# Performance work log

Measured on AMD Instinct MI355X. Metric: run time of the kernel, lower is better.

Reference implementation:

```python
import jax, jax.numpy as jnp
import numpy as np

B, N, D = 16, 1024, 128


def setup_inputs() -> dict:
    key = jax.random.key(0)
    ks = jax.random.split(key, 12)
    x = jax.random.normal(ks[0], (B, N, D), dtype=jnp.float32)
    # binary symmetric-ish adjacency mask (0/1 floats)
    adj = jax.random.randint(ks[1], (B, N, N), 0, 2).astype(jnp.float32)
    Ww = jax.random.normal(ks[2], (D, D), dtype=jnp.float32) * 0.05
    Wb = jax.random.normal(ks[3], (D,), dtype=jnp.float32) * 0.05
    A = jax.random.normal(ks[4], (D, D), dtype=jnp.float32) * 0.05
    wi_u = jax.random.normal(ks[5], (D,), dtype=jnp.float32) * 0.05
    wi_x = jax.random.normal(ks[6], (D,), dtype=jnp.float32) * 0.05
    wf_u = jax.random.normal(ks[7], (D,), dtype=jnp.float32) * 0.05
    wf_x = jax.random.normal(ks[8], (D,), dtype=jnp.float32) * 0.05
    wo_u = jax.random.normal(ks[9], (D,), dtype=jnp.float32) * 0.05
    wo_x = jax.random.normal(ks[10], (D,), dtype=jnp.float32) * 0.05
    return {"x": x, "adj": adj, "Ww": Ww, "Wb": Wb, "A": A,
            "wi_u": wi_u, "wi_x": wi_x, "wf_u": wf_u, "wf_x": wf_x,
            "wo_u": wo_u, "wo_x": wo_x}


def reference(x, adj, Ww, Wb, A, wi_u, wi_x, wf_u, wf_x, wo_u, wo_x):
    # h = W(x): [B,N,D]
    h = jnp.einsum('bnf,df->bnd', x, Ww) + Wb
    # e[b,j,k] = (h A) . h  -> symmetrized dense scores [B,N,N]
    e = jnp.einsum('bjl,bkl->bjk', jnp.einsum('bjd,dl->bjl', h, A), h)
    e = e + jnp.swapaxes(e, 1, 2)
    # masked softmax over axis=1 (columns), then re-mask by adj
    scores = jnp.where(adj > 0, e, 0.0)
    attention = jax.nn.softmax(scores, axis=1) * adj
    # aggregation
    h_prime = jax.nn.relu(jnp.einsum('bij,bjk->bik', attention, h))
    # LSTM-style gates: scalar per node, broadcast over features
    ic = jax.nn.sigmoid(h_prime @ wi_u + x @ wi_x)[..., None]
    fc = jax.nn.sigmoid(h_prime @ wf_u + x @ wf_x)[..., None]
    oc = jax.nn.sigmoid(h_prime @ wo_u + x @ wo_x)[..., None]
    return oc * jnp.tanh(ic * h_prime + fc * x)
```

## Files before the change

kernel.cpp:

```cpp
#include <hip/hip_runtime.h>


#define B_ 16
#define N_ 1024
#define D_ 128

typedef __attribute__((ext_vector_type(8))) short bf16x8;
typedef __attribute__((ext_vector_type(4))) float f32x4;

__device__ __forceinline__ unsigned short f2b(float f) {
    union { float f; unsigned int i; } v; v.f = f;
    unsigned int x = v.i;
    return (unsigned short)((x + 0x7fffu + ((x >> 16) & 1u)) >> 16);
}
__device__ __forceinline__ float clamp60(float v) {
    return fminf(fmaxf(v, -60.f), 60.f);
}
__device__ __forceinline__ bf16x8 load8f(const float* p) {
    float4 a = *reinterpret_cast<const float4*>(p);
    float4 b = *reinterpret_cast<const float4*>(p + 4);
    bf16x8 v;
    v[0] = (short)f2b(a.x); v[1] = (short)f2b(a.y);
    v[2] = (short)f2b(a.z); v[3] = (short)f2b(a.w);
    v[4] = (short)f2b(b.x); v[5] = (short)f2b(b.y);
    v[6] = (short)f2b(b.z); v[7] = (short)f2b(b.w);
    return v;
}

__global__ __launch_bounds__(256) void k0_w2t(
    const float* __restrict__ Ww, const float* __restrict__ Wb,
    const float* __restrict__ A, unsigned short* __restrict__ WwB,
    unsigned short* __restrict__ W2T, float* __restrict__ wbA) {
    int t = blockIdx.x * 256 + threadIdx.x;
    int l = t >> 7, f = t & 127;
    float acc = 0.f;
    for (int d = 0; d < 128; ++d)
        acc += A[d * 128 + l] * Ww[d * 128 + f];
    W2T[l * 128 + f] = f2b(acc);
    WwB[t] = f2b(Ww[t]);
    if (blockIdx.x == 0 && threadIdx.x < 128) {
        float s = 0.f;
        for (int d = 0; d < 128; ++d) s += Wb[d] * A[d * 128 + threadIdx.x];
        wbA[threadIdx.x] = s;
    }
}

__global__ __launch_bounds__(256) void kmask(
    const float* __restrict__ adj, unsigned long long* __restrict__ maskJ) {
    int w = threadIdx.x >> 6, lane = threadIdx.x & 63;
    size_t base = ((size_t)blockIdx.x * 4 + w) * 256;
    unsigned long long w0 = __ballot(adj[base + 0 * 64 + lane] > 0.f);
    unsigned long long w1 = __ballot(adj[base + 1 * 64 + lane] > 0.f);
    unsigned long long w2 = __ballot(adj[base + 2 * 64 + lane] > 0.f);
    unsigned long long w3 = __ballot(adj[base + 3 * 64 + lane] > 0.f);
    unsigned long long o = lane == 0 ? w0 : lane == 1 ? w1 : lane == 2 ? w2 : w3;
    if (lane < 4) maskJ[(base >> 6) + lane] = o;
}

__global__ __launch_bounds__(256) void k1_hu(
    const float* __restrict__ x, const unsigned short* __restrict__ WwB,
    const float* __restrict__ Wb, const unsigned short* __restrict__ W2T,
    const float* __restrict__ wbA,
    unsigned short* __restrict__ h, unsigned short* __restrict__ u,
    unsigned short* __restrict__ hT) {
    __shared__ unsigned short lds[16][128];
    int w = threadIdx.x >> 6, lane = threadIdx.x & 63;
    int c = lane & 15, q = lane >> 4;
    int rowbase = blockIdx.x * 16;
    int b = rowbase >> 10;
    int n0 = rowbase & 1023;

    bf16x8 xa[4];
    const float* xrow = x + (size_t)(rowbase + c) * 128;
#pragma unroll
    for (int ks = 0; ks < 4; ++ks)
        xa[ks] = load8f(xrow + ks * 32 + q * 8);

#pragma unroll
    for (int tt = 0; tt < 2; ++tt) {
        int t = w * 2 + tt;
        f32x4 acch = {0.f, 0.f, 0.f, 0.f};
        f32x4 accu = {0.f, 0.f, 0.f, 0.f};
        const unsigned short* wwrow = WwB + (t * 16 + c) * 128;
        const unsigned short* w2row = W2T + (t * 16 + c) * 128;
#pragma unroll
        for (int ks = 0; ks < 4; ++ks) {
            bf16x8 bw = *reinterpret_cast<const bf16x8*>(wwrow + ks * 32 + q * 8);
            bf16x8 b2 = *reinterpret_cast<const bf16x8*>(w2row + ks * 32 + q * 8);
            acch = __builtin_amdgcn_mfma_f32_16x16x32_bf16(xa[ks], bw, acch, 0, 0, 0);
            accu = __builtin_amdgcn_mfma_f32_16x16x32_bf16(xa[ks], b2, accu, 0, 0, 0);
        }
        float wb = Wb[t * 16 + c];
        float ub = wbA[t * 16 + c];
#pragma unroll
        for (int r = 0; r < 4; ++r) {
            int row = rowbase + q * 4 + r;
            unsigned short hv = f2b(acch[r] + wb);
            unsigned short uv = f2b(accu[r] + ub);
            h[(size_t)row * 128 + t * 16 + c] = hv;
            u[(size_t)row * 128 + t * 16 + c] = uv;
            lds[q * 4 + r][t * 16 + c] = hv;
        }
    }
    __syncthreads();
    int tid = threadIdx.x;
    if (tid < 128) {
        int d = tid;
        unsigned int p[8];
#pragma unroll
        for (int k = 0; k < 8; ++k) {
            unsigned int v0 = lds[2 * k][d], v1 = lds[2 * k + 1][d];
            p[k] = v0 | (v1 << 16);
        }
        size_t basehT = ((size_t)(b * 128 + d)) * 1024 + n0;
        uint4* dst = reinterpret_cast<uint4*>(hT + basehT);
        dst[0] = make_uint4(p[0], p[1], p[2], p[3]);
        dst[1] = make_uint4(p[4], p[5], p[6], p[7]);
    }
}


__global__ __launch_bounds__(256) void k2_scores(
    const unsigned short* __restrict__ h, const unsigned short* __restrict__ u,
    const unsigned long long* __restrict__ maskJ,
    float* __restrict__ att, float* __restrict__ colpart) {
    __shared__ unsigned long long lmask[16][16];
    int w = threadIdx.x >> 6, lane = threadIdx.x & 63;
    int c = lane & 15, q = lane >> 4;
    int b = blockIdx.x >> 6;
    int iblk = blockIdx.x & 63;
    int i0 = iblk * 16;
    const unsigned short* hb = h + (size_t)b * N_ * D_;
    const unsigned short* ub = u + (size_t)b * N_ * D_;

    lmask[threadIdx.x >> 4][threadIdx.x & 15] =
        maskJ[(size_t)(b * 1024 + i0 + (threadIdx.x >> 4)) * 16 + (threadIdx.x & 15)];
    __syncthreads();

    bf16x8 Au[4], Ah[4];
#pragma unroll
    for (int ks = 0; ks < 4; ++ks) {
        Au[ks] = *reinterpret_cast<const bf16x8*>(ub + (i0 + c) * 128 + ks * 32 + q * 8);
        Ah[ks] = *reinterpret_cast<const bf16x8*>(hb + (i0 + c) * 128 + ks * 32 + q * 8);
    }
    float* attrow = att + ((size_t)(b * 1024 + i0)) * 1024;
    float* cprow = colpart + ((size_t)(b * 64 + iblk)) * 1024;

    int jt0 = w * 16;
    bf16x8 Bh[2][4], Bu[2][4];
#pragma unroll
    for (int ks = 0; ks < 4; ++ks) {
        Bh[0][ks] = *reinterpret_cast<const bf16x8*>(hb + (jt0 * 16 + c) * 128 + ks * 32 + q * 8);
        Bu[0][ks] = *reinterpret_cast<const bf16x8*>(ub + (jt0 * 16 + c) * 128 + ks * 32 + q * 8);
    }
#pragma unroll
    for (int t = 0; t < 16; ++t) {
        int jt = jt0 + t, j0 = jt * 16;
        int cur = t & 1, nxt = cur ^ 1;
        if (t < 15) {
            int jn = (jt + 1) * 16;
#pragma unroll
            for (int ks = 0; ks < 4; ++ks) {
                Bh[nxt][ks] = *reinterpret_cast<const bf16x8*>(hb + (jn + c) * 128 + ks * 32 + q * 8);
                Bu[nxt][ks] = *reinterpret_cast<const bf16x8*>(ub + (jn + c) * 128 + ks * 32 + q * 8);
            }
        }
        f32x4 a1 = {0.f, 0.f, 0.f, 0.f};
        f32x4 a2 = {0.f, 0.f, 0.f, 0.f};
#pragma unroll
        for (int ks = 0; ks < 4; ++ks) {
            a1 = __builtin_amdgcn_mfma_f32_16x16x32_bf16(Au[ks], Bh[cur][ks], a1, 0, 0, 0);
            a2 = __builtin_amdgcn_mfma_f32_16x16x32_bf16(Ah[ks], Bu[cur][ks], a2, 0, 0, 0);
        }
        int wd = jt >> 2, sh = (jt & 3) * 16;
        float colp = 0.f;
#pragma unroll
        for (int r = 0; r < 4; ++r) {
            float e = a1[r] + a2[r];
            bool m = (lmask[q * 4 + r][wd] >> (sh + c)) & 1ull;
            float ex = m ? __expf(clamp60(e)) : 0.f;
            colp += m ? ex : 1.0f;
            attrow[(size_t)(q * 4 + r) * 1024 + j0 + c] = ex;
        }
        colp += __shfl_xor(colp, 16, 64);
        colp += __shfl_xor(colp, 32, 64);
        if (q == 0) cprow[j0 + c] = colp;
    }
}

__global__ __launch_bounds__(256) void k2b_recip(
    const float* __restrict__ colpart, float* __restrict__ rl0) {
    int g = blockIdx.x * 256 + threadIdx.x;
    int b = g >> 10, j = g & 1023;
    float s = 0.f;
    const float* p = colpart + (size_t)b * 64 * 1024 + j;
    for (int ib = 0; ib < 64; ++ib) s += p[(size_t)ib * 1024];
    rl0[g] = 1.0f / s;
}

__global__ __launch_bounds__(256) void k3_gemm(
    const float* __restrict__ att, const float* __restrict__ rl0,
    const unsigned short* __restrict__ hT, const float* __restrict__ x,
    const float* __restrict__ wi_u, const float* __restrict__ wi_x,
    const float* __restrict__ wf_u, const float* __restrict__ wf_x,
    const float* __restrict__ wo_u, const float* __restrict__ wo_x,
    float* __restrict__ out) {
    __shared__ float red[4][16][129];
    int w = threadIdx.x >> 6, lane = threadIdx.x & 63;
    int c = lane & 15, q = lane >> 4;
    int b = blockIdx.x >> 6;
    int i0 = (blockIdx.x & 63) * 16;
    const float* attrow = att + ((size_t)(b * 1024 + i0 + c)) * 1024;
    const unsigned short* hTb = hT + (size_t)b * 128 * 1024;
    const float* rl0b = rl0 + b * 1024;

    f32x4 hp[8];
#pragma unroll
    for (int t = 0; t < 8; ++t) hp[t] = (f32x4){0.f, 0.f, 0.f, 0.f};

#pragma unroll
    for (int tt = 0; tt < 8; ++tt) {
        int jp = w * 8 + tt;
        int jb = jp * 32 + q * 8;
        float4 e0 = *reinterpret_cast<const float4*>(attrow + jb);
        float4 e1 = *reinterpret_cast<const float4*>(attrow + jb + 4);
        float4 r0 = *reinterpret_cast<const float4*>(rl0b + jb);
        float4 r1 = *reinterpret_cast<const float4*>(rl0b + jb + 4);
        bf16x8 a;
        a[0] = (short)f2b(e0.x * r0.x); a[1] = (short)f2b(e0.y * r0.y);
        a[2] = (short)f2b(e0.z * r0.z); a[3] = (short)f2b(e0.w * r0.w);
        a[4] = (short)f2b(e1.x * r1.x); a[5] = (short)f2b(e1.y * r1.y);
        a[6] = (short)f2b(e1.z * r1.z); a[7] = (short)f2b(e1.w * r1.w);
#pragma unroll
        for (int t = 0; t < 8; ++t) {
            bf16x8 bt = *reinterpret_cast<const bf16x8*>(
                hTb + (size_t)(t * 16 + c) * 1024 + jp * 32 + q * 8);
            hp[t] = __builtin_amdgcn_mfma_f32_16x16x32_bf16(a, bt, hp[t], 0, 0, 0);
        }
    }

#pragma unroll
    for (int t = 0; t < 8; ++t)
#pragma unroll
        for (int r = 0; r < 4; ++r)
            red[w][q * 4 + r][t * 16 + c] = hp[t][r];
    __syncthreads();
    if (w != 0) return;

#pragma unroll
    for (int t = 0; t < 8; ++t)
#pragma unroll
        for (int r = 0; r < 4; ++r)
            hp[t][r] = red[0][q * 4 + r][t * 16 + c] + red[1][q * 4 + r][t * 16 + c]
                     + red[2][q * 4 + r][t * 16 + c] + red[3][q * 4 + r][t * 16 + c];

    float xv[8][4];
#pragma unroll
    for (int t = 0; t < 8; ++t)
#pragma unroll
        for (int r = 0; r < 4; ++r) {
            hp[t][r] = fmaxf(hp[t][r], 0.f);
            xv[t][r] = x[(size_t)(b * 1024 + i0 + q * 4 + r) * 128 + t * 16 + c];
        }
    float wiu[8], wix[8], wfu[8], wfx[8], wou[8], wox[8];
#pragma unroll
    for (int t = 0; t < 8; ++t) {
        wiu[t] = wi_u[t * 16 + c]; wix[t] = wi_x[t * 16 + c];
        wfu[t] = wf_u[t * 16 + c]; wfx[t] = wf_x[t * 16 + c];
        wou[t] = wo_u[t * 16 + c]; wox[t] = wo_x[t * 16 + c];
    }
#pragma unroll
    for (int r = 0; r < 4; ++r) {
        float zi = 0.f, zf = 0.f, zo = 0.f;
#pragma unroll
        for (int t = 0; t < 8; ++t) {
            zi += hp[t][r] * wiu[t] + xv[t][r] * wix[t];
            zf += hp[t][r] * wfu[t] + xv[t][r] * wfx[t];
            zo += hp[t][r] * wou[t] + xv[t][r] * wox[t];
        }
        zi += __shfl_xor(zi, 1, 64); zi += __shfl_xor(zi, 2, 64);
        zi += __shfl_xor(zi, 4, 64); zi += __shfl_xor(zi, 8, 64);
        zf += __shfl_xor(zf, 1, 64); zf += __shfl_xor(zf, 2, 64);
        zf += __shfl_xor(zf, 4, 64); zf += __shfl_xor(zf, 8, 64);
        zo += __shfl_xor(zo, 1, 64); zo += __shfl_xor(zo, 2, 64);
        zo += __shfl_xor(zo, 4, 64); zo += __shfl_xor(zo, 8, 64);
        float ic = 1.f / (1.f + __expf(-zi));
        float fc = 1.f / (1.f + __expf(-zf));
        float oc = 1.f / (1.f + __expf(-zo));
#pragma unroll
        for (int t = 0; t < 8; ++t) {
            float zz = ic * hp[t][r] + fc * xv[t][r];
            float th = 1.f - 2.f / (__expf(2.f * zz) + 1.f);
            out[(size_t)(b * 1024 + i0 + q * 4 + r) * 128 + t * 16 + c] = oc * th;
        }
    }
}

__global__ __launch_bounds__(256) void k2_stats(
    const unsigned short* __restrict__ h, const unsigned short* __restrict__ u,
    const unsigned long long* __restrict__ maskJ, float* __restrict__ rl0) {
    int w = threadIdx.x >> 6, lane = threadIdx.x & 63;
    int c = lane & 15, q = lane >> 4;
    int b = blockIdx.x >> 6;
    int j0 = (blockIdx.x & 63) * 16;
    const unsigned short* hb = h + (size_t)b * N_ * D_;
    const unsigned short* ub = u + (size_t)b * N_ * D_;

    bf16x8 Bh[4], Bu[4];
#pragma unroll
    for (int ks = 0; ks < 4; ++ks) {
        Bh[ks] = *reinterpret_cast<const bf16x8*>(hb + (j0 + c) * 128 + ks * 32 + q * 8);
        Bu[ks] = *reinterpret_cast<const bf16x8*>(ub + (j0 + c) * 128 + ks * 32 + q * 8);
    }
    float colsum = 0.f;
    const unsigned long long* mrow = maskJ + (size_t)b * 1024 * 16 + (j0 >> 6);
    int jb = j0 & 63;

    for (int it = w; it < 64; it += 4) {
        int i0 = it * 16;
        f32x4 acc = {0.f, 0.f, 0.f, 0.f};
#pragma unroll
        for (int ks = 0; ks < 4; ++ks) {
            bf16x8 au = *reinterpret_cast<const bf16x8*>(ub + (i0 + c) * 128 + ks * 32 + q * 8);
            bf16x8 ah = *reinterpret_cast<const bf16x8*>(hb + (i0 + c) * 128 + ks * 32 + q * 8);
            acc = __builtin_amdgcn_mfma_f32_16x16x32_bf16(au, Bh[ks], acc, 0, 0, 0);
            acc = __builtin_amdgcn_mfma_f32_16x16x32_bf16(ah, Bu[ks], acc, 0, 0, 0);
        }
#pragma unroll
        for (int r = 0; r < 4; ++r) {
            int i = i0 + q * 4 + r;
            unsigned long long mword = mrow[(size_t)i * 16];
            bool m = (mword >> (jb + c)) & 1ull;
            colsum += m ? __expf(clamp60(acc[r])) : 1.0f;
        }
    }
    colsum += __shfl_xor(colsum, 16, 64);
    colsum += __shfl_xor(colsum, 32, 64);
    __shared__ float part[4][16];
    if (lane < 16) part[w][lane] = colsum;
    __syncthreads();
    if (threadIdx.x < 16) {
        float s = part[0][threadIdx.x] + part[1][threadIdx.x]
                + part[2][threadIdx.x] + part[3][threadIdx.x];
        rl0[b * 1024 + j0 + threadIdx.x] = 1.0f / s;
    }
}

__global__ __launch_bounds__(256) void k3_fused(
    const unsigned short* __restrict__ h, const unsigned short* __restrict__ uu,
    const unsigned long long* __restrict__ maskJ, const float* __restrict__ rl0,
    const unsigned short* __restrict__ hT, const float* __restrict__ x,
    const float* __restrict__ wi_u, const float* __restrict__ wi_x,
    const float* __restrict__ wf_u, const float* __restrict__ wf_x,
    const float* __restrict__ wo_u, const float* __restrict__ wo_x,
    float* __restrict__ out) {
    __shared__ float red[4][16][129];
    int w = threadIdx.x >> 6, lane = threadIdx.x & 63;
    int c = lane & 15, q = lane >> 4;
    int b = blockIdx.x >> 6;
    int i0 = (blockIdx.x & 63) * 16;
    const unsigned short* hb = h + (size_t)b * N_ * D_;
    const unsigned short* ub = uu + (size_t)b * N_ * D_;
    const unsigned short* hTb = hT + (size_t)b * 128 * 1024;
    const unsigned long long* mrowI = maskJ + (size_t)(b * 1024 + i0 + c) * 16;
    const float* rl0b = rl0 + b * 1024;

    bf16x8 Bh[4], Bu[4];
#pragma unroll
    for (int ks = 0; ks < 4; ++ks) {
        Bh[ks] = *reinterpret_cast<const bf16x8*>(hb + (i0 + c) * 128 + ks * 32 + q * 8);
        Bu[ks] = *reinterpret_cast<const bf16x8*>(ub + (i0 + c) * 128 + ks * 32 + q * 8);
    }
    f32x4 hp[8];
#pragma unroll
    for (int t = 0; t < 8; ++t) hp[t] = (f32x4){0.f, 0.f, 0.f, 0.f};

    for (int jp = w; jp < 32; jp += 4) {
        int j0 = jp * 32;
        unsigned long long mw64 = mrowI[jp >> 1];
        unsigned int mbits = (unsigned int)(mw64 >> ((jp & 1) * 32));
        unsigned int u00, u01, u10, u11;
#pragma unroll
        for (int s = 0; s < 2; ++s) {
            int js = j0 + s * 16;
            f32x4 acc = {0.f, 0.f, 0.f, 0.f};
#pragma unroll
            for (int ks = 0; ks < 4; ++ks) {
                bf16x8 au = *reinterpret_cast<const bf16x8*>(ub + (js + c) * 128 + ks * 32 + q * 8);
                bf16x8 ah = *reinterpret_cast<const bf16x8*>(hb + (js + c) * 128 + ks * 32 + q * 8);
                acc = __builtin_amdgcn_mfma_f32_16x16x32_bf16(au, Bh[ks], acc, 0, 0, 0);
                acc = __builtin_amdgcn_mfma_f32_16x16x32_bf16(ah, Bu[ks], acc, 0, 0, 0);
            }
            float4 rv = *reinterpret_cast<const float4*>(rl0b + js + q * 4);
            int bb = s * 16 + q * 4;
            float a0 = ((mbits >> (bb + 0)) & 1u) ? __expf(clamp60(acc[0])) * rv.x : 0.f;
            float a1 = ((mbits >> (bb + 1)) & 1u) ? __expf(clamp60(acc[1])) * rv.y : 0.f;
            float a2 = ((mbits >> (bb + 2)) & 1u) ? __expf(clamp60(acc[2])) * rv.z : 0.f;
            float a3 = ((mbits >> (bb + 3)) & 1u) ? __expf(clamp60(acc[3])) * rv.w : 0.f;
            unsigned int p0 = (unsigned int)f2b(a0) | ((unsigned int)f2b(a1) << 16);
            unsigned int p1 = (unsigned int)f2b(a2) | ((unsigned int)f2b(a3) << 16);
            if (s == 0) { u00 = p0; u01 = p1; } else { u10 = p0; u11 = p1; }
        }
        int la = c + 32 * (q & 1);
        int lb = la + 16;
        unsigned int x0 = __shfl((int)u00, la, 64), x1 = __shfl((int)u01, la, 64);
        unsigned int x2 = __shfl((int)u00, lb, 64), x3 = __shfl((int)u01, lb, 64);
        unsigned int y0 = __shfl((int)u10, la, 64), y1 = __shfl((int)u11, la, 64);
        unsigned int y2 = __shfl((int)u10, lb, 64), y3 = __shfl((int)u11, lb, 64);
        bool hiq = (q >> 1) != 0;
        union { unsigned int ui[4]; bf16x8 v; } att;
        att.ui[0] = hiq ? y0 : x0;
        att.ui[1] = hiq ? y1 : x1;
        att.ui[2] = hiq ? y2 : x2;
        att.ui[3] = hiq ? y3 : x3;
#pragma unroll
        for (int t = 0; t < 8; ++t) {
            bf16x8 bt = *reinterpret_cast<const bf16x8*>(
                hTb + (size_t)(t * 16 + c) * 1024 + j0 + q * 8);
            hp[t] = __builtin_amdgcn_mfma_f32_16x16x32_bf16(att.v, bt, hp[t], 0, 0, 0);
        }
    }

#pragma unroll
    for (int t = 0; t < 8; ++t)
#pragma unroll
        for (int r = 0; r < 4; ++r)
            red[w][q * 4 + r][t * 16 + c] = hp[t][r];
    __syncthreads();
    if (w != 0) return;

#pragma unroll
    for (int t = 0; t < 8; ++t)
#pragma unroll
        for (int r = 0; r < 4; ++r)
            hp[t][r] = red[0][q * 4 + r][t * 16 + c] + red[1][q * 4 + r][t * 16 + c]
                     + red[2][q * 4 + r][t * 16 + c] + red[3][q * 4 + r][t * 16 + c];

    float xv[8][4];
#pragma unroll
    for (int t = 0; t < 8; ++t)
#pragma unroll
        for (int r = 0; r < 4; ++r) {
            hp[t][r] = fmaxf(hp[t][r], 0.f);
            xv[t][r] = x[(size_t)(b * 1024 + i0 + q * 4 + r) * 128 + t * 16 + c];
        }
    float wiu[8], wix[8], wfu[8], wfx[8], wou[8], wox[8];
#pragma unroll
    for (int t = 0; t < 8; ++t) {
        wiu[t] = wi_u[t * 16 + c]; wix[t] = wi_x[t * 16 + c];
        wfu[t] = wf_u[t * 16 + c]; wfx[t] = wf_x[t * 16 + c];
        wou[t] = wo_u[t * 16 + c]; wox[t] = wo_x[t * 16 + c];
    }
#pragma unroll
    for (int r = 0; r < 4; ++r) {
        float zi = 0.f, zf = 0.f, zo = 0.f;
#pragma unroll
        for (int t = 0; t < 8; ++t) {
            zi += hp[t][r] * wiu[t] + xv[t][r] * wix[t];
            zf += hp[t][r] * wfu[t] + xv[t][r] * wfx[t];
            zo += hp[t][r] * wou[t] + xv[t][r] * wox[t];
        }
        zi += __shfl_xor(zi, 1, 64); zi += __shfl_xor(zi, 2, 64);
        zi += __shfl_xor(zi, 4, 64); zi += __shfl_xor(zi, 8, 64);
        zf += __shfl_xor(zf, 1, 64); zf += __shfl_xor(zf, 2, 64);
        zf += __shfl_xor(zf, 4, 64); zf += __shfl_xor(zf, 8, 64);
        zo += __shfl_xor(zo, 1, 64); zo += __shfl_xor(zo, 2, 64);
        zo += __shfl_xor(zo, 4, 64); zo += __shfl_xor(zo, 8, 64);
        float ic = 1.f / (1.f + __expf(-zi));
        float fc = 1.f / (1.f + __expf(-zf));
        float oc = 1.f / (1.f + __expf(-zo));
#pragma unroll
        for (int t = 0; t < 8; ++t) {
            float zz = ic * hp[t][r] + fc * xv[t][r];
            float th = 1.f - 2.f / (__expf(2.f * zz) + 1.f);
            out[(size_t)(b * 1024 + i0 + q * 4 + r) * 128 + t * 16 + c] = oc * th;
        }
    }
}

extern "C" void kernel_launch(void* const* d_in, const int* in_sizes, int n_in,
                              void* d_out, int out_size, void* d_ws, size_t ws_size,
                              hipStream_t stream) {
    const float* x    = (const float*)d_in[0];
    const float* adj  = (const float*)d_in[1];
    const float* Ww   = (const float*)d_in[2];
    const float* Wb   = (const float*)d_in[3];
    const float* A    = (const float*)d_in[4];
    const float* wi_u = (const float*)d_in[5];
    const float* wi_x = (const float*)d_in[6];
    const float* wf_u = (const float*)d_in[7];
    const float* wf_x = (const float*)d_in[8];
    const float* wo_u = (const float*)d_in[9];
    const float* wo_x = (const float*)d_in[10];
    float* out = (float*)d_out;
    char* ws = (char*)d_ws;

    if (ws_size >= (84ull << 20)) {
        unsigned short* WwB = (unsigned short*)(ws);
        unsigned short* W2T = (unsigned short*)(ws + (32u << 10));
        float* wbA          = (float*)(ws + (64u << 10));
        float* rl0          = (float*)(ws + (128u << 10));
        unsigned long long* maskJ = (unsigned long long*)(ws + (256u << 10));
        float* colpart      = (float*)(ws + (4ull << 20));
        unsigned short* h   = (unsigned short*)(ws + (8ull << 20));
        unsigned short* u   = (unsigned short*)(ws + (12ull << 20));
        unsigned short* hT  = (unsigned short*)(ws + (16ull << 20));
        float* att          = (float*)(ws + (20ull << 20));

        k0_w2t<<<64, 256, 0, stream>>>(Ww, Wb, A, WwB, W2T, wbA);
        kmask<<<16384, 256, 0, stream>>>(adj, maskJ);
        k1_hu<<<1024, 256, 0, stream>>>(x, WwB, Wb, W2T, wbA, h, u, hT);
        k2_scores<<<1024, 256, 0, stream>>>(h, u, maskJ, att, colpart);
        k2b_recip<<<64, 256, 0, stream>>>(colpart, rl0);
        k3_gemm<<<1024, 256, 0, stream>>>(att, rl0, hT, x,
                                          wi_u, wi_x, wf_u, wf_x, wo_u, wo_x, out);
    } else {
        unsigned short* WwB = (unsigned short*)(ws);
        unsigned short* W2T = (unsigned short*)(ws + (32u << 10));
        float* wbA          = (float*)(ws + (64u << 10));
        float* rl0          = (float*)(ws + (128u << 10));
        unsigned short* h   = (unsigned short*)(ws + (1u << 20));
        unsigned short* u   = (unsigned short*)(ws + (5u << 20));
        unsigned short* hT  = (unsigned short*)(ws + (9u << 20));
        unsigned long long* maskJ = (unsigned long long*)(ws + (13u << 20));

        k0_w2t<<<64, 256, 0, stream>>>(Ww, Wb, A, WwB, W2T, wbA);
        kmask<<<16384, 256, 0, stream>>>(adj, maskJ);
        k1_hu<<<1024, 256, 0, stream>>>(x, WwB, Wb, W2T, wbA, h, u, hT);
        k2_stats<<<1024, 256, 0, stream>>>(h, u, maskJ, rl0);
        k3_fused<<<1024, 256, 0, stream>>>(h, u, maskJ, rl0, hT, x,
                                           wi_u, wi_x, wf_u, wf_x, wo_u, wo_x, out);
    }
}
```

Before: 253.3 us.

## Fuse adjacency mask into score kernel, store attention as bf16, split j halves

Drops the separate mask-packing kernel and has k2_scores ballot the adjacency directly for its row tile. The unnormalized attention intermediate is stored as bf16 instead of fp32, halving its write and read traffic between k2_scores and k3_gemm. The grid doubles by splitting the j range into two halves per block. The cost is one extra bf16 rounding on the exponentials before normalization, which can reduce accuracy.

```diff
diff --git a/kernel.cpp b/kernel.cpp
--- a/kernel.cpp
+++ b/kernel.cpp
@@ -8,6 +8,9 @@
 typedef __attribute__((ext_vector_type(8))) short bf16x8;
 typedef __attribute__((ext_vector_type(4))) float f32x4;
 
+__device__ __forceinline__ float b2f(unsigned short u) {
+    union { unsigned int i; float f; } v; v.i = ((unsigned int)u) << 16; return v.f;
+}
 __device__ __forceinline__ unsigned short f2b(float f) {
     union { float f; unsigned int i; } v; v.f = f;
     unsigned int x = v.i;
@@ -45,18 +48,6 @@
     }
 }
 
-__global__ __launch_bounds__(256) void kmask(
-    const float* __restrict__ adj, unsigned long long* __restrict__ maskJ) {
-    int w = threadIdx.x >> 6, lane = threadIdx.x & 63;
-    size_t base = ((size_t)blockIdx.x * 4 + w) * 256;
-    unsigned long long w0 = __ballot(adj[base + 0 * 64 + lane] > 0.f);
-    unsigned long long w1 = __ballot(adj[base + 1 * 64 + lane] > 0.f);
-    unsigned long long w2 = __ballot(adj[base + 2 * 64 + lane] > 0.f);
-    unsigned long long w3 = __ballot(adj[base + 3 * 64 + lane] > 0.f);
-    unsigned long long o = lane == 0 ? w0 : lane == 1 ? w1 : lane == 2 ? w2 : w3;
-    if (lane < 4) maskJ[(base >> 6) + lane] = o;
-}
-
 __global__ __launch_bounds__(256) void k1_hu(
     const float* __restrict__ x, const unsigned short* __restrict__ WwB,
     const float* __restrict__ Wb, const unsigned short* __restrict__ W2T,
@@ -122,20 +113,30 @@
 
 __global__ __launch_bounds__(256) void k2_scores(
     const unsigned short* __restrict__ h, const unsigned short* __restrict__ u,
-    const unsigned long long* __restrict__ maskJ,
-    float* __restrict__ att, float* __restrict__ colpart) {
-    __shared__ unsigned long long lmask[16][16];
+    const float* __restrict__ adj,
+    unsigned short* __restrict__ att, float* __restrict__ colpart) {
+    __shared__ unsigned long long lmask[16][8];
     int w = threadIdx.x >> 6, lane = threadIdx.x & 63;
     int c = lane & 15, q = lane >> 4;
-    int b = blockIdx.x >> 6;
-    int iblk = blockIdx.x & 63;
+    int b = blockIdx.x >> 7;
+    int iblk = (blockIdx.x >> 1) & 63;
+    int jh = blockIdx.x & 1;
     int i0 = iblk * 16;
+    int jbase = jh * 512;
     const unsigned short* hb = h + (size_t)b * N_ * D_;
     const unsigned short* ub = u + (size_t)b * N_ * D_;
 
-    lmask[threadIdx.x >> 4][threadIdx.x & 15] =
-        maskJ[(size_t)(b * 1024 + i0 + (threadIdx.x >> 4)) * 16 + (threadIdx.x & 15)];
-    __syncthreads();
+    {
+        const float* adjb = adj + ((size_t)(b * 1024 + i0 + w * 4)) * 1024 + jbase;
+#pragma unroll
+        for (int r = 0; r < 4; ++r) {
+#pragma unroll
+            for (int g = 0; g < 8; ++g) {
+                unsigned long long m = __ballot(adjb[(size_t)r * 1024 + g * 64 + lane] > 0.f);
+                if (lane == 0) lmask[w * 4 + r][g] = m;
+            }
+        }
+    }
 
     bf16x8 Au[4], Ah[4];
 #pragma unroll
@@ -143,22 +144,26 @@
         Au[ks] = *reinterpret_cast<const bf16x8*>(ub + (i0 + c) * 128 + ks * 32 + q * 8);
         Ah[ks] = *reinterpret_cast<const bf16x8*>(hb + (i0 + c) * 128 + ks * 32 + q * 8);
     }
-    float* attrow = att + ((size_t)(b * 1024 + i0)) * 1024;
+    __syncthreads();
+
+    unsigned short* attrow = att + ((size_t)(b * 1024 + i0)) * 1024;
     float* cprow = colpart + ((size_t)(b * 64 + iblk)) * 1024;
 
-    int jt0 = w * 16;
+    int jt0 = w * 8;
     bf16x8 Bh[2][4], Bu[2][4];
 #pragma unroll
     for (int ks = 0; ks < 4; ++ks) {
-        Bh[0][ks] = *reinterpret_cast<const bf16x8*>(hb + (jt0 * 16 + c) * 128 + ks * 32 + q * 8);
-        Bu[0][ks] = *reinterpret_cast<const bf16x8*>(ub + (jt0 * 16 + c) * 128 + ks * 32 + q * 8);
-    }
-#pragma unroll
-    for (int t = 0; t < 16; ++t) {
-        int jt = jt0 + t, j0 = jt * 16;
+        int jg = jbase + jt0 * 16;
+        Bh[0][ks] = *reinterpret_cast<const bf16x8*>(hb + (jg + c) * 128 + ks * 32 + q * 8);
+        Bu[0][ks] = *reinterpret_cast<const bf16x8*>(ub + (jg + c) * 128 + ks * 32 + q * 8);
+    }
+#pragma unroll
+    for (int t = 0; t < 8; ++t) {
+        int jtl = jt0 + t;
+        int j0g = jbase + jtl * 16;
         int cur = t & 1, nxt = cur ^ 1;
-        if (t < 15) {
-            int jn = (jt + 1) * 16;
+        if (t < 7) {
+            int jn = jbase + (jtl + 1) * 16;
 #pragma unroll
             for (int ks = 0; ks < 4; ++ks) {
                 Bh[nxt][ks] = *reinterpret_cast<const bf16x8*>(hb + (jn + c) * 128 + ks * 32 + q * 8);
@@ -172,7 +177,7 @@
             a1 = __builtin_amdgcn_mfma_f32_16x16x32_bf16(Au[ks], Bh[cur][ks], a1, 0, 0, 0);
             a2 = __builtin_amdgcn_mfma_f32_16x16x32_bf16(Ah[ks], Bu[cur][ks], a2, 0, 0, 0);
         }
-        int wd = jt >> 2, sh = (jt & 3) * 16;
+        int wd = jtl >> 2, sh = (jtl & 3) * 16;
         float colp = 0.f;
 #pragma unroll
         for (int r = 0; r < 4; ++r) {
@@ -180,11 +185,11 @@
             bool m = (lmask[q * 4 + r][wd] >> (sh + c)) & 1ull;
             float ex = m ? __expf(clamp60(e)) : 0.f;
             colp += m ? ex : 1.0f;
-            attrow[(size_t)(q * 4 + r) * 1024 + j0 + c] = ex;
+            attrow[(size_t)(q * 4 + r) * 1024 + j0g + c] = f2b(ex);
         }
         colp += __shfl_xor(colp, 16, 64);
         colp += __shfl_xor(colp, 32, 64);
-        if (q == 0) cprow[j0 + c] = colp;
+        if (q == 0) cprow[j0g + c] = colp;
     }
 }
 
@@ -199,7 +204,7 @@
 }
 
 __global__ __launch_bounds__(256) void k3_gemm(
-    const float* __restrict__ att, const float* __restrict__ rl0,
+    const unsigned short* __restrict__ att, const float* __restrict__ rl0,
     const unsigned short* __restrict__ hT, const float* __restrict__ x,
     const float* __restrict__ wi_u, const float* __restrict__ wi_x,
     const float* __restrict__ wf_u, const float* __restrict__ wf_x,
@@ -210,7 +215,7 @@
     int c = lane & 15, q = lane >> 4;
     int b = blockIdx.x >> 6;
     int i0 = (blockIdx.x & 63) * 16;
-    const float* attrow = att + ((size_t)(b * 1024 + i0 + c)) * 1024;
+    const unsigned short* attrow = att + ((size_t)(b * 1024 + i0 + c)) * 1024;
     const unsigned short* hTb = hT + (size_t)b * 128 * 1024;
     const float* rl0b = rl0 + b * 1024;
 
@@ -222,15 +227,18 @@
     for (int tt = 0; tt < 8; ++tt) {
         int jp = w * 8 + tt;
         int jb = jp * 32 + q * 8;
-        float4 e0 = *reinterpret_cast<const float4*>(attrow + jb);
-        float4 e1 = *reinterpret_cast<const float4*>(attrow + jb + 4);
+        bf16x8 eraw = *reinterpret_cast<const bf16x8*>(attrow + jb);
         float4 r0 = *reinterpret_cast<const float4*>(rl0b + jb);
         float4 r1 = *reinterpret_cast<const float4*>(rl0b + jb + 4);
         bf16x8 a;
-        a[0] = (short)f2b(e0.x * r0.x); a[1] = (short)f2b(e0.y * r0.y);
-        a[2] = (short)f2b(e0.z * r0.z); a[3] = (short)f2b(e0.w * r0.w);
-        a[4] = (short)f2b(e1.x * r1.x); a[5] = (short)f2b(e1.y * r1.y);
-        a[6] = (short)f2b(e1.z * r1.z); a[7] = (short)f2b(e1.w * r1.w);
+        a[0] = (short)f2b(b2f((unsigned short)eraw[0]) * r0.x);
+        a[1] = (short)f2b(b2f((unsigned short)eraw[1]) * r0.y);
+        a[2] = (short)f2b(b2f((unsigned short)eraw[2]) * r0.z);
+        a[3] = (short)f2b(b2f((unsigned short)eraw[3]) * r0.w);
+        a[4] = (short)f2b(b2f((unsigned short)eraw[4]) * r1.x);
+        a[5] = (short)f2b(b2f((unsigned short)eraw[5]) * r1.y);
+        a[6] = (short)f2b(b2f((unsigned short)eraw[6]) * r1.z);
+        a[7] = (short)f2b(b2f((unsigned short)eraw[7]) * r1.w);
 #pragma unroll
         for (int t = 0; t < 8; ++t) {
             bf16x8 bt = *reinterpret_cast<const bf16x8*>(
@@ -294,6 +302,18 @@
             out[(size_t)(b * 1024 + i0 + q * 4 + r) * 128 + t * 16 + c] = oc * th;
         }
     }
+}
+
+__global__ __launch_bounds__(256) void kmask(
+    const float* __restrict__ adj, unsigned long long* __restrict__ maskJ) {
+    int w = threadIdx.x >> 6, lane = threadIdx.x & 63;
+    size_t base = ((size_t)blockIdx.x * 4 + w) * 256;
+    unsigned long long w0 = __ballot(adj[base + 0 * 64 + lane] > 0.f);
+    unsigned long long w1 = __ballot(adj[base + 1 * 64 + lane] > 0.f);
+    unsigned long long w2 = __ballot(adj[base + 2 * 64 + lane] > 0.f);
+    unsigned long long w3 = __ballot(adj[base + 3 * 64 + lane] > 0.f);
+    unsigned long long o = lane == 0 ? w0 : lane == 1 ? w1 : lane == 2 ? w2 : w3;
+    if (lane < 4) maskJ[(base >> 6) + lane] = o;
 }
 
 __global__ __launch_bounds__(256) void k2_stats(
@@ -495,22 +515,20 @@
     float* out = (float*)d_out;
     char* ws = (char*)d_ws;
 
-    if (ws_size >= (84ull << 20)) {
+    if (ws_size >= (56ull << 20)) {
         unsigned short* WwB = (unsigned short*)(ws);
         unsigned short* W2T = (unsigned short*)(ws + (32u << 10));
         float* wbA          = (float*)(ws + (64u << 10));
         float* rl0          = (float*)(ws + (128u << 10));
-        unsigned long long* maskJ = (unsigned long long*)(ws + (256u << 10));
         float* colpart      = (float*)(ws + (4ull << 20));
         unsigned short* h   = (unsigned short*)(ws + (8ull << 20));
         unsigned short* u   = (unsigned short*)(ws + (12ull << 20));
         unsigned short* hT  = (unsigned short*)(ws + (16ull << 20));
-        float* att          = (float*)(ws + (20ull << 20));
+        unsigned short* att = (unsigned short*)(ws + (20ull << 20));
 
         k0_w2t<<<64, 256, 0, stream>>>(Ww, Wb, A, WwB, W2T, wbA);
-        kmask<<<16384, 256, 0, stream>>>(adj, maskJ);
         k1_hu<<<1024, 256, 0, stream>>>(x, WwB, Wb, W2T, wbA, h, u, hT);
-        k2_scores<<<1024, 256, 0, stream>>>(h, u, maskJ, att, colpart);
+        k2_scores<<<2048, 256, 0, stream>>>(h, u, adj, att, colpart);
         k2b_recip<<<64, 256, 0, stream>>>(colpart, rl0);
         k3_gemm<<<1024, 256, 0, stream>>>(att, rl0, hT, x,
                                           wi_u, wi_x, wf_u, wf_x, wo_u, wo_x, out);
```

Result: slower. 273.1 us (+7.8%).

## Store unnormalized attention in bf16 and restructure score B-operand prefetch

Applied to the files above, without the earlier changes.

The intermediate exp-score matrix written by the score kernel and read by the aggregation GEMM is stored as bf16 instead of fp32, halving its 64MB round trip through memory. The aggregation kernel widens the bf16 values back to float before scaling by the column reciprocal and re-rounding. The score kernel's double-buffered B-operand loads now prefetch two tiles ahead and are issued after the MFMAs so the freed slot is reused. The workspace threshold for the fast path is lowered to match the smaller buffer. The cost is a double bf16 rounding of attention weights, which adds some numerical error.

```diff
diff --git a/kernel.cpp b/kernel.cpp
--- a/kernel.cpp
+++ b/kernel.cpp
@@ -8,6 +8,9 @@
 typedef __attribute__((ext_vector_type(8))) short bf16x8;
 typedef __attribute__((ext_vector_type(4))) float f32x4;
 
+__device__ __forceinline__ float b2f(unsigned short u) {
+    union { unsigned int i; float f; } v; v.i = ((unsigned int)u) << 16; return v.f;
+}
 __device__ __forceinline__ unsigned short f2b(float f) {
     union { float f; unsigned int i; } v; v.f = f;
     unsigned int x = v.i;
@@ -123,7 +126,7 @@
 __global__ __launch_bounds__(256) void k2_scores(
     const unsigned short* __restrict__ h, const unsigned short* __restrict__ u,
     const unsigned long long* __restrict__ maskJ,
-    float* __restrict__ att, float* __restrict__ colpart) {
+    unsigned short* __restrict__ att, float* __restrict__ colpart) {
     __shared__ unsigned long long lmask[16][16];
     int w = threadIdx.x >> 6, lane = threadIdx.x & 63;
     int c = lane & 15, q = lane >> 4;
@@ -143,34 +146,38 @@
         Au[ks] = *reinterpret_cast<const bf16x8*>(ub + (i0 + c) * 128 + ks * 32 + q * 8);
         Ah[ks] = *reinterpret_cast<const bf16x8*>(hb + (i0 + c) * 128 + ks * 32 + q * 8);
     }
-    float* attrow = att + ((size_t)(b * 1024 + i0)) * 1024;
+    unsigned short* attrow = att + ((size_t)(b * 1024 + i0)) * 1024;
     float* cprow = colpart + ((size_t)(b * 64 + iblk)) * 1024;
 
     int jt0 = w * 16;
     bf16x8 Bh[2][4], Bu[2][4];
 #pragma unroll
-    for (int ks = 0; ks < 4; ++ks) {
-        Bh[0][ks] = *reinterpret_cast<const bf16x8*>(hb + (jt0 * 16 + c) * 128 + ks * 32 + q * 8);
-        Bu[0][ks] = *reinterpret_cast<const bf16x8*>(ub + (jt0 * 16 + c) * 128 + ks * 32 + q * 8);
+    for (int s = 0; s < 2; ++s) {
+        int jg = (jt0 + s) * 16;
+#pragma unroll
+        for (int ks = 0; ks < 4; ++ks) {
+            Bh[s][ks] = *reinterpret_cast<const bf16x8*>(hb + (jg + c) * 128 + ks * 32 + q * 8);
+            Bu[s][ks] = *reinterpret_cast<const bf16x8*>(ub + (jg + c) * 128 + ks * 32 + q * 8);
+        }
     }
 #pragma unroll
     for (int t = 0; t < 16; ++t) {
         int jt = jt0 + t, j0 = jt * 16;
-        int cur = t & 1, nxt = cur ^ 1;
-        if (t < 15) {
-            int jn = (jt + 1) * 16;
-#pragma unroll
-            for (int ks = 0; ks < 4; ++ks) {
-                Bh[nxt][ks] = *reinterpret_cast<const bf16x8*>(hb + (jn + c) * 128 + ks * 32 + q * 8);
-                Bu[nxt][ks] = *reinterpret_cast<const bf16x8*>(ub + (jn + c) * 128 + ks * 32 + q * 8);
-            }
-        }
+        int slot = t & 1;
         f32x4 a1 = {0.f, 0.f, 0.f, 0.f};
         f32x4 a2 = {0.f, 0.f, 0.f, 0.f};
 #pragma unroll
         for (int ks = 0; ks < 4; ++ks) {
-            a1 = __builtin_amdgcn_mfma_f32_16x16x32_bf16(Au[ks], Bh[cur][ks], a1, 0, 0, 0);
-            a2 = __builtin_amdgcn_mfma_f32_16x16x32_bf16(Ah[ks], Bu[cur][ks], a2, 0, 0, 0);
+            a1 = __builtin_amdgcn_mfma_f32_16x16x32_bf16(Au[ks], Bh[slot][ks], a1, 0, 0, 0);
+            a2 = __builtin_amdgcn_mfma_f32_16x16x32_bf16(Ah[ks], Bu[slot][ks], a2, 0, 0, 0);
+        }
+        if (t < 14) {
+            int jn = (jt + 2) * 16;
+#pragma unroll
+            for (int ks = 0; ks < 4; ++ks) {
+                Bh[slot][ks] = *reinterpret_cast<const bf16x8*>(hb + (jn + c) * 128 + ks * 32 + q * 8);
+                Bu[slot][ks] = *reinterpret_cast<const bf16x8*>(ub + (jn + c) * 128 + ks * 32 + q * 8);
+            }
         }
         int wd = jt >> 2, sh = (jt & 3) * 16;
         float colp = 0.f;
@@ -180,7 +187,7 @@
             bool m = (lmask[q * 4 + r][wd] >> (sh + c)) & 1ull;
             float ex = m ? __expf(clamp60(e)) : 0.f;
             colp += m ? ex : 1.0f;
-            attrow[(size_t)(q * 4 + r) * 1024 + j0 + c] = ex;
+            attrow[(size_t)(q * 4 + r) * 1024 + j0 + c] = f2b(ex);
         }
         colp += __shfl_xor(colp, 16, 64);
         colp += __shfl_xor(colp, 32, 64);
@@ -199,7 +206,7 @@
 }
 
 __global__ __launch_bounds__(256) void k3_gemm(
-    const float* __restrict__ att, const float* __restrict__ rl0,
+    const unsigned short* __restrict__ att, const float* __restrict__ rl0,
     const unsigned short* __restrict__ hT, const float* __restrict__ x,
     const float* __restrict__ wi_u, const float* __restrict__ wi_x,
     const float* __restrict__ wf_u, const float* __restrict__ wf_x,
@@ -210,7 +217,7 @@
     int c = lane & 15, q = lane >> 4;
     int b = blockIdx.x >> 6;
     int i0 = (blockIdx.x & 63) * 16;
-    const float* attrow = att + ((size_t)(b * 1024 + i0 + c)) * 1024;
+    const unsigned short* attrow = att + ((size_t)(b * 1024 + i0 + c)) * 1024;
     const unsigned short* hTb = hT + (size_t)b * 128 * 1024;
     const float* rl0b = rl0 + b * 1024;
 
@@ -222,15 +229,18 @@
     for (int tt = 0; tt < 8; ++tt) {
         int jp = w * 8 + tt;
         int jb = jp * 32 + q * 8;
-        float4 e0 = *reinterpret_cast<const float4*>(attrow + jb);
-        float4 e1 = *reinterpret_cast<const float4*>(attrow + jb + 4);
+        bf16x8 eraw = *reinterpret_cast<const bf16x8*>(attrow + jb);
         float4 r0 = *reinterpret_cast<const float4*>(rl0b + jb);
         float4 r1 = *reinterpret_cast<const float4*>(rl0b + jb + 4);
         bf16x8 a;
-        a[0] = (short)f2b(e0.x * r0.x); a[1] = (short)f2b(e0.y * r0.y);
-        a[2] = (short)f2b(e0.z * r0.z); a[3] = (short)f2b(e0.w * r0.w);
-        a[4] = (short)f2b(e1.x * r1.x); a[5] = (short)f2b(e1.y * r1.y);
-        a[6] = (short)f2b(e1.z * r1.z); a[7] = (short)f2b(e1.w * r1.w);
+        a[0] = (short)f2b(b2f((unsigned short)eraw[0]) * r0.x);
+        a[1] = (short)f2b(b2f((unsigned short)eraw[1]) * r0.y);
+        a[2] = (short)f2b(b2f((unsigned short)eraw[2]) * r0.z);
+        a[3] = (short)f2b(b2f((unsigned short)eraw[3]) * r0.w);
+        a[4] = (short)f2b(b2f((unsigned short)eraw[4]) * r1.x);
+        a[5] = (short)f2b(b2f((unsigned short)eraw[5]) * r1.y);
+        a[6] = (short)f2b(b2f((unsigned short)eraw[6]) * r1.z);
+        a[7] = (short)f2b(b2f((unsigned short)eraw[7]) * r1.w);
 #pragma unroll
         for (int t = 0; t < 8; ++t) {
             bf16x8 bt = *reinterpret_cast<const bf16x8*>(
@@ -495,7 +505,7 @@
     float* out = (float*)d_out;
     char* ws = (char*)d_ws;
 
-    if (ws_size >= (84ull << 20)) {
+    if (ws_size >= (56ull << 20)) {
         unsigned short* WwB = (unsigned short*)(ws);
         unsigned short* W2T = (unsigned short*)(ws + (32u << 10));
         float* wbA          = (float*)(ws + (64u << 10));
@@ -505,7 +515,7 @@
         unsigned short* h   = (unsigned short*)(ws + (8ull << 20));
         unsigned short* u   = (unsigned short*)(ws + (12ull << 20));
         unsigned short* hT  = (unsigned short*)(ws + (16ull << 20));
-        float* att          = (float*)(ws + (20ull << 20));
+        unsigned short* att = (unsigned short*)(ws + (20ull << 20));
 
         k0_w2t<<<64, 256, 0, stream>>>(Ww, Wb, A, WwB, W2T, wbA);
         kmask<<<16384, 256, 0, stream>>>(adj, maskJ);
```

Result: no change. 249.9 us (-1.4%).
